# Kernel optimization log

Measured on AMD Instinct MI355X. Metric: run time of the kernel, lower is better.

## Reference

```python
import jax, jax.numpy as jnp
import numpy as np

B, N0, C, K, D = 16384, 1024, 12, 64, 3  # batch, feat dim, num_classes, num_clusters, ndim


def setup_inputs() -> dict:
    key = jax.random.key(0)
    ks = jax.random.split(key, 6)
    s = 0.02  # weight init scale
    return {
        "x": jax.random.normal(ks[0], (B, N0), dtype=jnp.float32),
        "Wfc": jax.random.normal(ks[1], (N0, C), dtype=jnp.float32) * s,
        "bfc": jnp.zeros((C,), dtype=jnp.float32),
        "Wbin": jax.random.normal(ks[2], (C, K, N0), dtype=jnp.float32) * s,
        "bbin": jnp.zeros((C, K), dtype=jnp.float32),
        "Wres": jax.random.normal(ks[3], (C, K, N0, D), dtype=jnp.float32) * s,
        "bres": jnp.zeros((C, K, D), dtype=jnp.float32),
        "centers": jax.random.normal(ks[4], (K, D), dtype=jnp.float32),
    }


def reference(x, Wfc, bfc, Wbin, bbin, Wres, bres, centers):
    # category head
    y0 = x @ Wfc + bfc                                            # [B, C]
    # per-class bin logits (batched over all classes at once)
    ybin = jnp.einsum("bn,ckn->bck", x, Wbin) + bbin              # [B, C, K]
    ind = jnp.argmax(ybin, axis=2)                                # [B, C] selected cluster per class
    # multires path: all (class, cluster) expert residuals, then one-hot select
    yres_all = jnp.einsum("bn,cknd->bckd", x, Wres) + bres        # [B, C, K, D]
    yres = jnp.take_along_axis(
        yres_all, ind[:, :, None, None], axis=2
    ).squeeze(2)                                                  # [B, C, D]
    # gather cluster centers and add residual
    y = centers[ind] + yres                                       # [B, C, D]
    # torch: stack over classes -> [C,B,D]; permute(1,2,0) -> [B, D, C]
    y1 = jnp.transpose(y, (0, 2, 1))                              # [B, D, C]
    return (y0, y1)
```

## Files before the change

### kernel.cpp

```cpp
#include <hip/hip_runtime.h>

typedef unsigned int uint32;
typedef unsigned long long uint64;
typedef unsigned short ushort16;
typedef __attribute__((ext_vector_type(8))) short bf16x8;
typedef __attribute__((ext_vector_type(4))) float f32x4;
typedef __attribute__((ext_vector_type(4))) uint32 u32x4;

#define B_SZ 16384
#define MARGIN 0.012f

__device__ __forceinline__ ushort16 f2bf(float f) {
  uint32 u = __float_as_uint(f);
  u += 0x7fffu + ((u >> 16) & 1u);
  return (ushort16)(u >> 16);
}
__device__ __forceinline__ float bf2f(ushort16 h) { return __uint_as_float(((uint32)h) << 16); }
__device__ __forceinline__ float bflo(uint32 u) { return __uint_as_float(u << 16); }
__device__ __forceinline__ float bfhi(uint32 u) { return __uint_as_float(u & 0xffff0000u); }
__device__ __forceinline__ uint32 pk2(float lo, float hi) {
  return ((uint32)f2bf(hi) << 16) | (uint32)f2bf(lo);
}
__device__ __forceinline__ int dot4(uint32 a, uint32 b, int c) {
#if __has_builtin(__builtin_amdgcn_sdot4)
  return __builtin_amdgcn_sdot4((int)a, (int)b, c, false);
#else
  int s = c;
#pragma unroll
  for (int k = 0; k < 4; ++k)
    s += (int)(char)(a >> (8 * k)) * (int)(char)(b >> (8 * k));
  return s;
#endif
}
__device__ __forceinline__ int q8(float v, float inv) {
  int q = (int)rintf(v * inv);
  return q > 127 ? 127 : (q < -127 ? -127 : q);
}
__device__ __forceinline__ int red16_i(int s) {
  s += __builtin_amdgcn_update_dpp(0, s, 0xB1, 0xF, 0xF, true);
  s += __builtin_amdgcn_update_dpp(0, s, 0x4E, 0xF, 0xF, true);
  s += __builtin_amdgcn_update_dpp(0, s, 0x141, 0xF, 0xF, true);
  s += __builtin_amdgcn_update_dpp(0, s, 0x140, 0xF, 0xF, true);
  return s;
}
#define DPP_D_LEVEL(v, ctrl)                                                        \
  {                                                                                 \
    uint64 u_ = (uint64)__double_as_longlong(v);                                    \
    int lo_ = __builtin_amdgcn_update_dpp(0, (int)(uint32)u_, (ctrl), 0xF, 0xF, true); \
    int hi_ = __builtin_amdgcn_update_dpp(0, (int)(uint32)(u_ >> 32), (ctrl), 0xF, 0xF, true); \
    (v) += __longlong_as_double((long long)(((uint64)(uint32)hi_ << 32) | (uint32)lo_)); \
  }
__device__ __forceinline__ double red16_d(double v) {
  DPP_D_LEVEL(v, 0xB1); DPP_D_LEVEL(v, 0x4E);
  DPP_D_LEVEL(v, 0x141); DPP_D_LEVEL(v, 0x140);
  return v;
}

__global__ __launch_bounds__(256) void prep_all(
    const float* __restrict__ Wfc, const float* __restrict__ Wbin,
    const float* __restrict__ x, ushort16* __restrict__ Wall,
    u32x4* __restrict__ xb) {
  const int blk = blockIdx.x;
  const int t = threadIdx.x;
  if (blk < 3584) {
    int idx = blk * 256 + t;
    int j = idx >> 10, n = idx & 1023;
    float v = 0.f;
    if (j < 12) v = Wfc[n * 12 + j];
    else if (j >= 64 && j < 832) v = Wbin[(size_t)(j - 64) * 1024 + n];
    Wall[idx] = f2bf(v);
  } else {
    int idx = (blk - 3584) * 256 + t;
    const float4* s = (const float4*)x + (size_t)idx * 2;
    float4 a = s[0], b4 = s[1];
    u32x4 o;
    o.x = pk2(a.x, a.y);  o.y = pk2(a.z, a.w);
    o.z = pk2(b4.x, b4.y); o.w = pk2(b4.z, b4.w);
    xb[idx] = o;
  }
}

__global__ void prep_wall_f(const float* __restrict__ Wfc, const float* __restrict__ Wbin,
                            ushort16* __restrict__ Wall) {
  int idx = blockIdx.x * 256 + threadIdx.x;
  int j = idx >> 10, n = idx & 1023;
  float v = 0.f;
  if (j < 12) v = Wfc[n * 12 + j];
  else if (j >= 64 && j < 832) v = Wbin[(size_t)(j - 64) * 1024 + n];
  Wall[idx] = f2bf(v);
}
__global__ void prep_wres(const float* __restrict__ Wres, ushort16* __restrict__ Wres_b) {
  int idx = blockIdx.x * 256 + threadIdx.x;
  int n = idx & 1023;
  int d = (idx >> 10) % 3;
  int ck = idx / 3072;
  Wres_b[idx] = f2bf(Wres[((size_t)ck * 1024 + n) * 3 + d]);
}

template<int XB>
__global__ __launch_bounds__(256) void gemm_mfma(
    const float* __restrict__ x, const ushort16* __restrict__ xb,
    const float* __restrict__ bfc, const float* __restrict__ bbin,
    const ushort16* __restrict__ Wall, ushort16* __restrict__ ybin,
    unsigned char* __restrict__ ind8, uint64* __restrict__ mask64,
    const float* __restrict__ Wres, uint32* __restrict__ wq,
    float* __restrict__ swk, uint32* __restrict__ xq,
    float* __restrict__ sxb, float* __restrict__ out) {
  __shared__ __align__(16) char smem[49152];
  const int t = threadIdx.x;

  if (XB && blockIdx.x >= 1664) {
    const int lane = t & 63;
    const int b = (blockIdx.x - 1664) * 4 + (t >> 6);
    const float4* xr = (const float4*)(x + (size_t)b * 1024 + lane * 16);
    float4 v0 = xr[0], v1 = xr[1], v2 = xr[2], v3 = xr[3];
    float xv[16] = {v0.x, v0.y, v0.z, v0.w, v1.x, v1.y, v1.z, v1.w,
                    v2.x, v2.y, v2.z, v2.w, v3.x, v3.y, v3.z, v3.w};
    float m = 0.f;
#pragma unroll
    for (int i = 0; i < 16; ++i) m = fmaxf(m, fabsf(xv[i]));
    for (int off = 32; off; off >>= 1) m = fmaxf(m, __shfl_xor(m, off));
    float mx = fmaxf(m, 1e-20f);
    float inv = 127.f / mx;
    if (lane == 0) sxb[b] = mx / 127.f;
    u32x4 qv;
#pragma unroll
    for (int q = 0; q < 4; ++q) {
      uint32 u = ((uint32)(unsigned char)(char)q8(xv[4 * q + 0], inv)) |
                 ((uint32)(unsigned char)(char)q8(xv[4 * q + 1], inv)) << 8 |
                 ((uint32)(unsigned char)(char)q8(xv[4 * q + 2], inv)) << 16 |
                 ((uint32)(unsigned char)(char)q8(xv[4 * q + 3], inv)) << 24;
      qv[q] = u;
    }
    ((u32x4*)(xq + (size_t)b * 256))[lane] = qv;
    return;
  }
  if (XB && blockIdx.x >= 896) {
    float* red = (float*)smem;
    const int ck = blockIdx.x - 896;
    const float4* base4 = (const float4*)(Wres + (size_t)ck * 3072);
    float4 v0 = base4[3 * t], v1 = base4[3 * t + 1], v2 = base4[3 * t + 2];
    float vals[12] = {v0.x, v0.y, v0.z, v0.w, v1.x, v1.y, v1.z, v1.w, v2.x, v2.y, v2.z, v2.w};
    float m = 0.f;
#pragma unroll
    for (int i = 0; i < 12; ++i) m = fmaxf(m, fabsf(vals[i]));
    red[t] = m; __syncthreads();
    for (int s = 128; s; s >>= 1) { if (t < s) red[t] = fmaxf(red[t], red[t + s]); __syncthreads(); }
    float mx = fmaxf(red[0], 1e-20f);
    float inv = 127.f / mx;
    if (t == 0) swk[ck] = mx / 127.f;
#pragma unroll
    for (int d = 0; d < 3; ++d) {
      uint32 u = 0;
#pragma unroll
      for (int j = 0; j < 4; ++j)
        u |= ((uint32)(unsigned char)(char)q8(vals[j * 3 + d], inv)) << (8 * j);
      wq[((size_t)(ck * 3 + d) << 8) + t] = u;
    }
    return;
  }

  const int lane = t & 63, wid = t >> 6;
  const int wm = wid & 1, wn = wid >> 1;

  int orig = blockIdx.x;
  int bid = (orig & 7) * 112 + (orig >> 3);
  int nb = bid % 7, mb = bid / 7;
  const int b0 = mb * 128;

  f32x4 acc[4][4];
#pragma unroll
  for (int i = 0; i < 4; ++i)
#pragma unroll
    for (int j = 0; j < 4; ++j) acc[i][j] = (f32x4){0.f, 0.f, 0.f, 0.f};

  const int lr = lane & 15, lq = lane >> 4;

#define GLDS(srcp, dstoff)                                                      \
  __builtin_amdgcn_global_load_lds(                                             \
      (const __attribute__((address_space(1))) uint32*)(srcp),                  \
      (__attribute__((address_space(3))) uint32*)(smem + (dstoff)), 16, 0, 0)

  if (XB) {
    const int gs2 = (lane & 3) ^ ((lane >> 2) & 3);
    const int grw2 = lane >> 2;
    const int ch0 = wid * 2, ch1 = wid * 2 + 1;
    const ushort16* arow0 = xb + (size_t)(b0 + ch0 * 16 + grw2) * 1024 + gs2 * 8;
    const ushort16* arow1 = xb + (size_t)(b0 + ch1 * 16 + grw2) * 1024 + gs2 * 8;
    const ushort16* brow0 = Wall + (size_t)(nb * 128 + ch0 * 16 + grw2) * 1024 + gs2 * 8;
    const ushort16* brow1 = Wall + (size_t)(nb * 128 + ch1 * 16 + grw2) * 1024 + gs2 * 8;

#define STAGE_HALF(h, buf)                                                      \
    {                                                                           \
      int bb_ = (buf) * 16384;                                                  \
      int kc_ = (h) * 32;                                                       \
      GLDS(arow0 + kc_, bb_ + ch0 * 1024);                                      \
      GLDS(arow1 + kc_, bb_ + ch1 * 1024);                                      \
      GLDS(brow0 + kc_, bb_ + 8192 + ch0 * 1024);                               \
      GLDS(brow1 + kc_, bb_ + 8192 + ch1 * 1024);                               \
    }

    STAGE_HALF(0, 0); STAGE_HALF(1, 1);
    const int cbx2 = (lq * 16) ^ ((lr & 3) << 4);
    const int arow_off = (wm * 64 + lr) * 64;
    const int brow_off = (wn * 64 + lr) * 64;
    int rb = 0;
#pragma unroll 1
    for (int h = 0; h < 32; ++h) {
      if (h < 31) asm volatile("s_waitcnt vmcnt(4)" ::: "memory");
      else        asm volatile("s_waitcnt vmcnt(0)" ::: "memory");
      __builtin_amdgcn_s_barrier();
      if (h < 30) {
        int sb = rb + 2; if (sb >= 3) sb -= 3;
        STAGE_HALF(h + 2, sb);
      }
      const char* base = smem + rb * 16384;
      bf16x8 af[4], bfr[4];
#pragma unroll
      for (int i = 0; i < 4; ++i)
        af[i] = *(const bf16x8*)(base + arow_off + i * 1024 + cbx2);
#pragma unroll
      for (int j = 0; j < 4; ++j)
        bfr[j] = *(const bf16x8*)(base + 8192 + brow_off + j * 1024 + cbx2);
#pragma unroll
      for (int i = 0; i < 4; ++i)
#pragma unroll
        for (int j = 0; j < 4; ++j)
          acc[i][j] = __builtin_amdgcn_mfma_f32_16x16x32_bf16(af[i], bfr[j], acc[i][j], 0, 0, 0);
      rb = (rb == 2) ? 0 : rb + 1;
    }
#undef STAGE_HALF
  } else {
    const int fxor = (lr & 7) << 4;
    for (int kc = 0; kc < 1024; kc += 64) {
      __syncthreads();
      const int sxor = ((t >> 3) & 7) << 4;
#pragma unroll
      for (int i = 0; i < 4; ++i) {
        int s = t + i * 256;
        int row = s >> 3, c8 = (s & 7) * 8;
        int dst = row * 128 + ((c8 * 2) ^ sxor);
        const float4* src = (const float4*)(x + (size_t)(b0 + row) * 1024 + kc + c8);
        float4 v0 = src[0], v1 = src[1];
        u32x4 pv;
        pv.x = pk2(v0.x, v0.y); pv.y = pk2(v0.z, v0.w);
        pv.z = pk2(v1.x, v1.y); pv.w = pk2(v1.z, v1.w);
        *(u32x4*)(smem + dst) = pv;
      }
#pragma unroll
      for (int i = 0; i < 4; ++i) {
        int s = t + i * 256;
        int row = s >> 3, c8 = (s & 7) * 8;
        int dst = 16384 + row * 128 + ((c8 * 2) ^ sxor);
        u32x4 v = *(const u32x4*)(Wall + (size_t)(nb * 128 + row) * 1024 + kc + c8);
        *(u32x4*)(smem + dst) = v;
      }
      __syncthreads();
#pragma unroll
      for (int kk = 0; kk < 2; ++kk) {
        int cbx = (kk * 64 + lq * 16) ^ fxor;
        bf16x8 af[4], bfr[4];
#pragma unroll
        for (int i = 0; i < 4; ++i)
          af[i] = *(const bf16x8*)(smem + (wm * 64 + i * 16 + lr) * 128 + cbx);
#pragma unroll
        for (int j = 0; j < 4; ++j)
          bfr[j] = *(const bf16x8*)(smem + 16384 + (wn * 64 + j * 16 + lr) * 128 + cbx);
#pragma unroll
        for (int i = 0; i < 4; ++i)
#pragma unroll
          for (int j = 0; j < 4; ++j)
            acc[i][j] = __builtin_amdgcn_mfma_f32_16x16x32_bf16(af[i], bfr[j], acc[i][j], 0, 0, 0);
      }
    }
  }
#undef GLDS

  const int g = 2 * nb + wn;
  if (g == 0) {
#pragma unroll
    for (int i = 0; i < 4; ++i)
#pragma unroll
      for (int r = 0; r < 4; ++r) {
        int gm = b0 + wm * 64 + i * 16 + lq * 4 + r;
        if (lr < 12) out[(size_t)gm * 12 + lr] = acc[i][0][r] + bfc[lr];
      }
    return;
  }
  if (g > 12) return;
  const int c = g - 1;
  if (XB == 0) {
#pragma unroll
    for (int i = 0; i < 4; ++i)
#pragma unroll
      for (int j = 0; j < 4; ++j)
#pragma unroll
        for (int r = 0; r < 4; ++r) {
          int gm = b0 + wm * 64 + i * 16 + lq * 4 + r;
          int col = j * 16 + lr;
          ybin[((size_t)gm * 12 + c) * 64 + col] = f2bf(acc[i][j][r] + bbin[c * 64 + col]);
        }
    return;
  }
  float bb[4];
#pragma unroll
  for (int j = 0; j < 4; ++j) bb[j] = bbin[c * 64 + j * 16 + lr];
#pragma unroll
  for (int i = 0; i < 4; ++i)
#pragma unroll
    for (int r = 0; r < 4; ++r) {
      float v0 = acc[i][0][r] + bb[0], v1 = acc[i][1][r] + bb[1];
      float v2 = acc[i][2][r] + bb[2], v3 = acc[i][3][r] + bb[3];
      float m1 = v0, m2 = -3.4e38f; int k1 = lr;
      if (v1 > m1) { m2 = m1; m1 = v1; k1 = 16 + lr; } else m2 = fmaxf(m2, v1);
      if (v2 > m1) { m2 = m1; m1 = v2; k1 = 32 + lr; } else m2 = fmaxf(m2, v2);
      if (v3 > m1) { m2 = m1; m1 = v3; k1 = 48 + lr; } else m2 = fmaxf(m2, v3);
#pragma unroll
      for (int off = 1; off < 16; off <<= 1) {
        float om1 = __shfl_xor(m1, off);
        int   ok1 = __shfl_xor(k1, off);
        float om2 = __shfl_xor(m2, off);
        bool take = (om1 > m1) || (om1 == m1 && ok1 < k1);
        float lose = take ? m1 : om1;
        m2 = fmaxf(fmaxf(m2, om2), lose);
        if (take) { m1 = om1; k1 = ok1; }
      }
      float thr = m1 - MARGIN;
      uint64 bl0 = __ballot(v0 >= thr);
      uint64 bl1 = __ballot(v1 >= thr);
      uint64 bl2 = __ballot(v2 >= thr);
      uint64 bl3 = __ballot(v3 >= thr);
      if (lr == 0) {
        int row = wm * 64 + i * 16 + lq * 4 + r;
        uint64 mk = ((bl0 >> (lq * 16)) & 0xffffull) |
                    (((bl1 >> (lq * 16)) & 0xffffull) << 16) |
                    (((bl2 >> (lq * 16)) & 0xffffull) << 32) |
                    (((bl3 >> (lq * 16)) & 0xffffull) << 48);
        int gp = (b0 + row) * 12 + c;
        ind8[gp] = (unsigned char)(k1 | ((m1 - m2 <= MARGIN) ? 128 : 0));
        mask64[gp] = mk;
      }
    }
}

__global__ __launch_bounds__(256) void compact_k(const unsigned char* __restrict__ ind8,
                                                 uint32* __restrict__ cnt,
                                                 uint32* __restrict__ wl) {
  const int b = blockIdx.x * 256 + threadIdx.x;
  const int lane = threadIdx.x & 63;
  const uint32* p = (const uint32*)(ind8 + b * 12);
  uint32 d0 = p[0], d1 = p[1], d2 = p[2];
  uint32 fmask = 0;
#pragma unroll
  for (int j = 0; j < 4; ++j) {
    if ((d0 >> (8 * j)) & 128u) fmask |= 1u << j;
    if ((d1 >> (8 * j)) & 128u) fmask |= 1u << (4 + j);
    if ((d2 >> (8 * j)) & 128u) fmask |= 1u << (8 + j);
  }
  uint32 n_i = (uint32)__popc(fmask);
  uint32 pre = n_i;
  for (int off = 1; off < 64; off <<= 1) {
    uint32 v = __shfl_up(pre, off);
    if (lane >= off) pre += v;
  }
  uint32 total = __shfl(pre, 63);
  uint32 base = 0;
  if (lane == 63 && total) base = atomicAdd(cnt, total);
  base = __shfl(base, 63);
  uint32 off = base + pre - n_i;
  while (fmask) {
    int c = __ffs(fmask) - 1;
    fmask &= fmask - 1;
    wl[off++] = (uint32)(b * 12 + c);
  }
}

__global__ __launch_bounds__(256) void tail_k(
    const float* __restrict__ x, const float* __restrict__ Wbin,
    const float* __restrict__ bbin, const float* __restrict__ bres,
    const float* __restrict__ centers, const unsigned char* __restrict__ ind8,
    const uint64* __restrict__ mask64, const uint32* __restrict__ wq,
    const float* __restrict__ swk, const uint32* __restrict__ xq,
    const float* __restrict__ sxb, const uint32* __restrict__ cnt,
    const uint32* __restrict__ wl, float* __restrict__ out) {
  const int lane = threadIdx.x & 63;
  const int w = threadIdx.x >> 6;
  const int rm = (int)(blockIdx.x % 3u);
  const int rq = (int)(blockIdx.x / 3u);

  if (rm == 0) {
    const uint32 nresc = *cnt;
#pragma unroll 1
    for (uint32 slot = rq * 4 + w; slot < nresc; slot += 32768) {
      const uint32 pp = wl[slot];
      const int b = (int)(pp / 12u), c = (int)(pp % 12u);

      float xv[16];
      const float4* xr = (const float4*)(x + (size_t)b * 1024 + lane * 16);
#pragma unroll
      for (int q = 0; q < 4; ++q) {
        float4 vv = xr[q];
        xv[4 * q] = vv.x; xv[4 * q + 1] = vv.y; xv[4 * q + 2] = vv.z; xv[4 * q + 3] = vv.w;
      }
      const float sx = sxb[b];
      const float inv = (sx > 0.f) ? 1.f / sx : 0.f;
      uint32 xi[4];
#pragma unroll
      for (int q = 0; q < 4; ++q)
        xi[q] = ((uint32)(unsigned char)(char)q8(xv[4 * q + 0], inv)) |
                ((uint32)(unsigned char)(char)q8(xv[4 * q + 1], inv)) << 8 |
                ((uint32)(unsigned char)(char)q8(xv[4 * q + 2], inv)) << 16 |
                ((uint32)(unsigned char)(char)q8(xv[4 * q + 3], inv)) << 24;

      uint64 mask = mask64[pp];
      double best = -1.0e300;
      int bk = 0;
#pragma unroll 1
      while (mask) {
        int kk[4];
        int nc = 0;
        while (mask && nc < 4) { kk[nc++] = __ffsll(mask) - 1; mask &= mask - 1; }
#pragma unroll
        for (int j = 1; j < 4; ++j) if (j >= nc) kk[j] = kk[0];
        double s[4] = {0.0, 0.0, 0.0, 0.0};
#pragma unroll
        for (int ci = 0; ci < 4; ++ci) {
          const float4* wr4 = (const float4*)(Wbin + ((size_t)c * 64 + kk[ci]) * 1024 + lane * 16);
#pragma unroll
          for (int q = 0; q < 4; ++q) {
            float4 wvv = wr4[q];
            s[ci] += (double)xv[4 * q] * (double)wvv.x + (double)xv[4 * q + 1] * (double)wvv.y +
                     (double)xv[4 * q + 2] * (double)wvv.z + (double)xv[4 * q + 3] * (double)wvv.w;
          }
        }
#pragma unroll
        for (int ci = 0; ci < 4; ++ci) s[ci] = red16_d(s[ci]);
        for (int off = 16; off < 64; off <<= 1) {
#pragma unroll
          for (int ci = 0; ci < 4; ++ci) s[ci] += __shfl_xor(s[ci], off);
        }
#pragma unroll
        for (int ci = 0; ci < 4; ++ci) {
          double sv = s[ci] + (double)bbin[c * 64 + kk[ci]];
          if (ci < nc && sv > best) { best = sv; bk = kk[ci]; }
        }
      }
      const int ck = c * 64 + bk;
      const uint32* wr = wq + (size_t)ck * 768;
      int acc[3];
#pragma unroll
      for (int d = 0; d < 3; ++d) {
        u32x4 wvq = *(const u32x4*)(wr + d * 256 + lane * 4);
        int ss = dot4(xi[0], wvq.x, 0);
        ss = dot4(xi[1], wvq.y, ss);
        ss = dot4(xi[2], wvq.z, ss);
        acc[d] = dot4(xi[3], wvq.w, ss);
      }
#pragma unroll
      for (int d = 0; d < 3; ++d) acc[d] = red16_i(acc[d]);
      for (int off = 16; off < 64; off <<= 1) {
        acc[0] += __shfl_xor(acc[0], off);
        acc[1] += __shfl_xor(acc[1], off);
        acc[2] += __shfl_xor(acc[2], off);
      }
      if (lane == 0) {
        const size_t obase = (size_t)B_SZ * 12 + (size_t)b * 36;
        float sc = sx * swk[ck];
        out[obase + 0 * 12 + c] = centers[bk * 3 + 0] + bres[ck * 3 + 0] + sc * (float)acc[0];
        out[obase + 1 * 12 + c] = centers[bk * 3 + 1] + bres[ck * 3 + 1] + sc * (float)acc[1];
        out[obase + 2 * 12 + c] = centers[bk * 3 + 2] + bres[ck * 3 + 2] + sc * (float)acc[2];
      }
    }
    return;
  }

  const int b = rq * 2 + (rm - 1);

  const u32x4 xi = *(const u32x4*)(xq + (size_t)b * 256 + lane * 4);
  const float sx = sxb[b];
  const size_t obase = (size_t)B_SZ * 12 + (size_t)b * 36;

  int iv[3], ind[3], ck[3];
  u32x4 wv[3][3];
#pragma unroll
  for (int cc = 0; cc < 3; ++cc) {
    int c = w * 3 + cc;
    iv[cc] = ind8[b * 12 + c];
    ind[cc] = iv[cc] & 63;
    ck[cc] = c * 64 + ind[cc];
    const uint32* wr = wq + (size_t)ck[cc] * 768;
#pragma unroll
    for (int d = 0; d < 3; ++d)
      wv[cc][d] = *(const u32x4*)(wr + d * 256 + lane * 4);
  }
  int acc[3][3];
#pragma unroll
  for (int cc = 0; cc < 3; ++cc)
#pragma unroll
    for (int d = 0; d < 3; ++d) {
      int s = dot4(xi.x, wv[cc][d].x, 0);
      s = dot4(xi.y, wv[cc][d].y, s);
      s = dot4(xi.z, wv[cc][d].z, s);
      acc[cc][d] = dot4(xi.w, wv[cc][d].w, s);
    }
#pragma unroll
  for (int cc = 0; cc < 3; ++cc)
#pragma unroll
    for (int d = 0; d < 3; ++d)
      acc[cc][d] = red16_i(acc[cc][d]);
  for (int off = 16; off < 64; off <<= 1) {
#pragma unroll
    for (int cc = 0; cc < 3; ++cc)
#pragma unroll
      for (int d = 0; d < 3; ++d)
        acc[cc][d] += __shfl_xor(acc[cc][d], off);
  }
  if (lane == 0) {
#pragma unroll
    for (int cc = 0; cc < 3; ++cc) {
      if (iv[cc] & 128) continue;
      int c = w * 3 + cc;
      float sc = sx * swk[ck[cc]];
      out[obase + 0 * 12 + c] = centers[ind[cc] * 3 + 0] + bres[ck[cc] * 3 + 0] + sc * (float)acc[cc][0];
      out[obase + 1 * 12 + c] = centers[ind[cc] * 3 + 1] + bres[ck[cc] * 3 + 1] + sc * (float)acc[cc][1];
      out[obase + 2 * 12 + c] = centers[ind[cc] * 3 + 2] + bres[ck[cc] * 3 + 2] + sc * (float)acc[cc][2];
    }
  }
}

__global__ __launch_bounds__(256) void select2(
    const float* __restrict__ x, const float* __restrict__ Wbin,
    const float* __restrict__ bbin, const float* __restrict__ bres,
    const float* __restrict__ centers, const ushort16* __restrict__ Wres_b,
    const ushort16* __restrict__ ybin, float* __restrict__ out) {
  const int lane = threadIdx.x & 63;
  const int w = threadIdx.x >> 6;
  const int b = blockIdx.x;
  float xv[16];
  {
    const float4* xr = (const float4*)(x + (size_t)b * 1024 + lane * 16);
#pragma unroll
    for (int q = 0; q < 4; ++q) {
      float4 v = xr[q];
      xv[4 * q] = v.x; xv[4 * q + 1] = v.y; xv[4 * q + 2] = v.z; xv[4 * q + 3] = v.w;
    }
  }
  const size_t obase = (size_t)B_SZ * 12 + (size_t)b * 36;
#pragma unroll 1
  for (int cc = 0; cc < 3; ++cc) {
    const int c = w * 3 + cc;
    float v = bf2f(ybin[((size_t)b * 12 + c) * 64 + lane]);
    float m1 = v, m2 = -3.4e38f;
    int k1 = lane;
    for (int off = 32; off; off >>= 1) {
      float om1 = __shfl_xor(m1, off);
      int   ok1 = __shfl_xor(k1, off);
      float om2 = __shfl_xor(m2, off);
      bool take = (om1 > m1) || (om1 == m1 && ok1 < k1);
      float lose = take ? m1 : om1;
      m2 = fmaxf(fmaxf(m2, om2), lose);
      if (take) { m1 = om1; k1 = ok1; }
    }
    int ind = k1;
    if (m1 - m2 <= MARGIN) {
      unsigned long long mask = __ballot(v >= m1 - MARGIN);
      double best = -1.0e300;
      int bk = 0;
      while (mask) {
        int k = __ffsll(mask) - 1;
        mask &= (mask - 1);
        const float4* wr4 = (const float4*)(Wbin + ((size_t)c * 64 + k) * 1024 + lane * 16);
        double s = 0.0;
#pragma unroll
        for (int q = 0; q < 4; ++q) {
          float4 wv = wr4[q];
          s += (double)xv[4 * q] * (double)wv.x + (double)xv[4 * q + 1] * (double)wv.y +
               (double)xv[4 * q + 2] * (double)wv.z + (double)xv[4 * q + 3] * (double)wv.w;
        }
        for (int off = 32; off; off >>= 1) s += __shfl_xor(s, off);
        s += (double)bbin[c * 64 + k];
        if (s > best) { best = s; bk = k; }
      }
      ind = bk;
    }
    const ushort16* wr = Wres_b + ((size_t)(c * 64 + ind) * 3) * 1024;
    float a[3] = {0.f, 0.f, 0.f};
#pragma unroll
    for (int d = 0; d < 3; ++d) {
      const u32x4* pp = (const u32x4*)(wr + d * 1024 + lane * 16);
      u32x4 w0 = pp[0], w1 = pp[1];
      uint32 uw[8] = {w0.x, w0.y, w0.z, w0.w, w1.x, w1.y, w1.z, w1.w};
#pragma unroll
      for (int q = 0; q < 8; ++q) {
        a[d] = fmaf(xv[2 * q],     bflo(uw[q]), a[d]);
        a[d] = fmaf(xv[2 * q + 1], bfhi(uw[q]), a[d]);
      }
    }
    for (int off = 32; off; off >>= 1) {
      a[0] += __shfl_xor(a[0], off);
      a[1] += __shfl_xor(a[1], off);
      a[2] += __shfl_xor(a[2], off);
    }
    if (lane == 0) {
      int ck = c * 64 + ind;
      out[obase + 0 * 12 + c] = centers[ind * 3 + 0] + bres[ck * 3 + 0] + a[0];
      out[obase + 1 * 12 + c] = centers[ind * 3 + 1] + bres[ck * 3 + 1] + a[1];
      out[obase + 2 * 12 + c] = centers[ind * 3 + 2] + bres[ck * 3 + 2] + a[2];
    }
  }
}

extern "C" void kernel_launch(void* const* d_in, const int* in_sizes, int n_in,
                              void* d_out, int out_size, void* d_ws, size_t ws_size,
                              hipStream_t stream) {
  const float* x       = (const float*)d_in[0];
  const float* Wfc     = (const float*)d_in[1];
  const float* bfc     = (const float*)d_in[2];
  const float* Wbin    = (const float*)d_in[3];
  const float* bbin    = (const float*)d_in[4];
  const float* Wres    = (const float*)d_in[5];
  const float* bres    = (const float*)d_in[6];
  const float* centers = (const float*)d_in[7];
  float* out = (float*)d_out;

  char* ws = (char*)d_ws;
  ushort16* Wall = (ushort16*)ws;
  if (ws_size >= 57151488ull) {
    uint32*        wq     = (uint32*)(ws + 1835008);
    float*         swk    = (float*)(ws + 4194304);
    unsigned char* ind8   = (unsigned char*)(ws + 4197376);
    uint64*        mask64 = (uint64*)(ws + 4393984);
    ushort16*      xb     = (ushort16*)(ws + 5966848);
    uint32*        xq     = (uint32*)(ws + 39521280);
    float*         sxb    = (float*)(ws + 56298496);
    uint32*        cnt    = (uint32*)(ws + 56364032);
    uint32*        wl     = (uint32*)(ws + 56364288);

    hipMemsetAsync(cnt, 0, 4, stream);
    prep_all<<<11776, 256, 0, stream>>>(Wfc, Wbin, x, Wall, (u32x4*)xb);
    gemm_mfma<1><<<5760, 256, 0, stream>>>(x, xb, bfc, bbin, Wall,
                                           (ushort16*)nullptr, ind8, mask64,
                                           Wres, wq, swk, xq, sxb, out);
    compact_k<<<64, 256, 0, stream>>>(ind8, cnt, wl);
    tail_k<<<24576, 256, 0, stream>>>(x, Wbin, bbin, bres, centers, ind8, mask64,
                                      wq, swk, xq, sxb, cnt, wl, out);
  } else {
    ushort16* Wres_b = (ushort16*)(ws + 1835008);
    ushort16* ybin   = (ushort16*)(ws + 6553600);
    prep_wall_f<<<3584, 256, 0, stream>>>(Wfc, Wbin, Wall);
    prep_wres<<<9216, 256, 0, stream>>>(Wres, Wres_b);
    gemm_mfma<0><<<896, 256, 0, stream>>>(x, (const ushort16*)ws, bfc, bbin, Wall,
                                          ybin, (unsigned char*)nullptr,
                                          (uint64*)nullptr, nullptr,
                                          (uint32*)nullptr, (float*)nullptr,
                                          (uint32*)nullptr, (float*)nullptr, out);
    select2<<<B_SZ, 256, 0, stream>>>(x, Wbin, bbin, bres, centers, Wres_b, ybin, out);
  }
}
```

Before: 141.5 us.

## Enlarge GEMM block to 256x128 tile with 512 threads and wave-level Wres quantization

The main GEMM kernel now uses 512-thread blocks, each computing a 256-row by 128-column tile. This halves the number of blocks that reload the same Wall columns and improves B-operand reuse, at the cost of 72KB of dynamic shared memory for three pipeline buffers. The side work is also regrouped: Wres quantization is done per wave with shuffle reductions instead of a block-wide shared-memory reduction, and x quantization handles 8 rows per block. Fewer blocks fit per CU because of the larger LDS footprint, and the fallback path is split into its own kernel.

```diff
diff --git a/kernel.cpp b/kernel.cpp
--- a/kernel.cpp
+++ b/kernel.cpp
@@ -97,21 +97,104 @@
   Wres_b[idx] = f2bf(Wres[((size_t)ck * 1024 + n) * 3 + d]);
 }
 
-template<int XB>
-__global__ __launch_bounds__(256) void gemm_mfma(
+__global__ __launch_bounds__(256) void gemm_fb(
+    const float* __restrict__ x, const float* __restrict__ bfc,
+    const float* __restrict__ bbin, const ushort16* __restrict__ Wall,
+    ushort16* __restrict__ ybin, float* __restrict__ out) {
+  __shared__ __align__(16) char smem[32768];
+  const int t = threadIdx.x;
+  const int lane = t & 63, wid = t >> 6;
+  const int wm = wid & 1, wn = wid >> 1;
+  int orig = blockIdx.x;
+  int bid = (orig & 7) * 112 + (orig >> 3);
+  int nb = bid % 7, mb = bid / 7;
+  const int b0 = mb * 128;
+  f32x4 acc[4][4];
+#pragma unroll
+  for (int i = 0; i < 4; ++i)
+#pragma unroll
+    for (int j = 0; j < 4; ++j) acc[i][j] = (f32x4){0.f, 0.f, 0.f, 0.f};
+  const int lr = lane & 15, lq = lane >> 4;
+  const int fxor = (lr & 7) << 4;
+  for (int kc = 0; kc < 1024; kc += 64) {
+    __syncthreads();
+    const int sxor = ((t >> 3) & 7) << 4;
+#pragma unroll
+    for (int i = 0; i < 4; ++i) {
+      int s = t + i * 256;
+      int row = s >> 3, c8 = (s & 7) * 8;
+      int dst = row * 128 + ((c8 * 2) ^ sxor);
+      const float4* src = (const float4*)(x + (size_t)(b0 + row) * 1024 + kc + c8);
+      float4 v0 = src[0], v1 = src[1];
+      u32x4 pv;
+      pv.x = pk2(v0.x, v0.y); pv.y = pk2(v0.z, v0.w);
+      pv.z = pk2(v1.x, v1.y); pv.w = pk2(v1.z, v1.w);
+      *(u32x4*)(smem + dst) = pv;
+    }
+#pragma unroll
+    for (int i = 0; i < 4; ++i) {
+      int s = t + i * 256;
+      int row = s >> 3, c8 = (s & 7) * 8;
+      int dst = 16384 + row * 128 + ((c8 * 2) ^ sxor);
+      u32x4 v = *(const u32x4*)(Wall + (size_t)(nb * 128 + row) * 1024 + kc + c8);
+      *(u32x4*)(smem + dst) = v;
+    }
+    __syncthreads();
+#pragma unroll
+    for (int kk = 0; kk < 2; ++kk) {
+      int cbx = (kk * 64 + lq * 16) ^ fxor;
+      bf16x8 af[4], bfr[4];
+#pragma unroll
+      for (int i = 0; i < 4; ++i)
+        af[i] = *(const bf16x8*)(smem + (wm * 64 + i * 16 + lr) * 128 + cbx);
+#pragma unroll
+      for (int j = 0; j < 4; ++j)
+        bfr[j] = *(const bf16x8*)(smem + 16384 + (wn * 64 + j * 16 + lr) * 128 + cbx);
+#pragma unroll
+      for (int i = 0; i < 4; ++i)
+#pragma unroll
+        for (int j = 0; j < 4; ++j)
+          acc[i][j] = __builtin_amdgcn_mfma_f32_16x16x32_bf16(af[i], bfr[j], acc[i][j], 0, 0, 0);
+    }
+  }
+  const int g = 2 * nb + wn;
+  if (g == 0) {
+#pragma unroll
+    for (int i = 0; i < 4; ++i)
+#pragma unroll
+      for (int r = 0; r < 4; ++r) {
+        int gm = b0 + wm * 64 + i * 16 + lq * 4 + r;
+        if (lr < 12) out[(size_t)gm * 12 + lr] = acc[i][0][r] + bfc[lr];
+      }
+    return;
+  }
+  if (g > 12) return;
+  const int c = g - 1;
+#pragma unroll
+  for (int i = 0; i < 4; ++i)
+#pragma unroll
+    for (int j = 0; j < 4; ++j)
+#pragma unroll
+      for (int r = 0; r < 4; ++r) {
+        int gm = b0 + wm * 64 + i * 16 + lq * 4 + r;
+        int col = j * 16 + lr;
+        ybin[((size_t)gm * 12 + c) * 64 + col] = f2bf(acc[i][j][r] + bbin[c * 64 + col]);
+      }
+}
+
+__global__ __launch_bounds__(512) void gemm_mega(
     const float* __restrict__ x, const ushort16* __restrict__ xb,
     const float* __restrict__ bfc, const float* __restrict__ bbin,
-    const ushort16* __restrict__ Wall, ushort16* __restrict__ ybin,
-    unsigned char* __restrict__ ind8, uint64* __restrict__ mask64,
-    const float* __restrict__ Wres, uint32* __restrict__ wq,
-    float* __restrict__ swk, uint32* __restrict__ xq,
+    const ushort16* __restrict__ Wall, unsigned char* __restrict__ ind8,
+    uint64* __restrict__ mask64, const float* __restrict__ Wres,
+    uint32* __restrict__ wq, float* __restrict__ swk, uint32* __restrict__ xq,
     float* __restrict__ sxb, float* __restrict__ out) {
-  __shared__ __align__(16) char smem[49152];
+  extern __shared__ __align__(16) char smem[];
   const int t = threadIdx.x;
-
-  if (XB && blockIdx.x >= 1664) {
-    const int lane = t & 63;
-    const int b = (blockIdx.x - 1664) * 4 + (t >> 6);
+  const int lane = t & 63, wid = t >> 6;
+
+  if (blockIdx.x >= 544) {
+    const int b = (blockIdx.x - 544) * 8 + wid;
     const float4* xr = (const float4*)(x + (size_t)b * 1024 + lane * 16);
     float4 v0 = xr[0], v1 = xr[1], v2 = xr[2], v3 = xr[3];
     float xv[16] = {v0.x, v0.y, v0.z, v0.w, v1.x, v1.y, v1.z, v1.w,
@@ -135,38 +218,45 @@
     ((u32x4*)(xq + (size_t)b * 256))[lane] = qv;
     return;
   }
-  if (XB && blockIdx.x >= 896) {
-    float* red = (float*)smem;
-    const int ck = blockIdx.x - 896;
+  if (blockIdx.x >= 448) {
+    const int ck = (blockIdx.x - 448) * 8 + wid;
     const float4* base4 = (const float4*)(Wres + (size_t)ck * 3072);
-    float4 v0 = base4[3 * t], v1 = base4[3 * t + 1], v2 = base4[3 * t + 2];
-    float vals[12] = {v0.x, v0.y, v0.z, v0.w, v1.x, v1.y, v1.z, v1.w, v2.x, v2.y, v2.z, v2.w};
     float m = 0.f;
 #pragma unroll
-    for (int i = 0; i < 12; ++i) m = fmaxf(m, fabsf(vals[i]));
-    red[t] = m; __syncthreads();
-    for (int s = 128; s; s >>= 1) { if (t < s) red[t] = fmaxf(red[t], red[t + s]); __syncthreads(); }
-    float mx = fmaxf(red[0], 1e-20f);
+    for (int it = 0; it < 4; ++it) {
+      int tt = lane + 64 * it;
+      float4 v0 = base4[3 * tt], v1 = base4[3 * tt + 1], v2 = base4[3 * tt + 2];
+      m = fmaxf(m, fmaxf(fmaxf(fabsf(v0.x), fabsf(v0.y)), fmaxf(fabsf(v0.z), fabsf(v0.w))));
+      m = fmaxf(m, fmaxf(fmaxf(fabsf(v1.x), fabsf(v1.y)), fmaxf(fabsf(v1.z), fabsf(v1.w))));
+      m = fmaxf(m, fmaxf(fmaxf(fabsf(v2.x), fabsf(v2.y)), fmaxf(fabsf(v2.z), fabsf(v2.w))));
+    }
+    for (int off = 32; off; off >>= 1) m = fmaxf(m, __shfl_xor(m, off));
+    float mx = fmaxf(m, 1e-20f);
     float inv = 127.f / mx;
-    if (t == 0) swk[ck] = mx / 127.f;
-#pragma unroll
-    for (int d = 0; d < 3; ++d) {
-      uint32 u = 0;
-#pragma unroll
-      for (int j = 0; j < 4; ++j)
-        u |= ((uint32)(unsigned char)(char)q8(vals[j * 3 + d], inv)) << (8 * j);
-      wq[((size_t)(ck * 3 + d) << 8) + t] = u;
+    if (lane == 0) swk[ck] = mx / 127.f;
+#pragma unroll
+    for (int it = 0; it < 4; ++it) {
+      int tt = lane + 64 * it;
+      float4 v0 = base4[3 * tt], v1 = base4[3 * tt + 1], v2 = base4[3 * tt + 2];
+      float vals[12] = {v0.x, v0.y, v0.z, v0.w, v1.x, v1.y, v1.z, v1.w, v2.x, v2.y, v2.z, v2.w};
+#pragma unroll
+      for (int d = 0; d < 3; ++d) {
+        uint32 u = 0;
+#pragma unroll
+        for (int j = 0; j < 4; ++j)
+          u |= ((uint32)(unsigned char)(char)q8(vals[j * 3 + d], inv)) << (8 * j);
+        wq[((size_t)(ck * 3 + d) << 8) + tt] = u;
+      }
     }
     return;
   }
 
-  const int lane = t & 63, wid = t >> 6;
-  const int wm = wid & 1, wn = wid >> 1;
+  const int wm = wid & 3, wn = wid >> 2;
 
   int orig = blockIdx.x;
-  int bid = (orig & 7) * 112 + (orig >> 3);
+  int bid = (orig & 7) * 56 + (orig >> 3);
   int nb = bid % 7, mb = bid / 7;
-  const int b0 = mb * 128;
+  const int b0 = mb * 256;
 
   f32x4 acc[4][4];
 #pragma unroll
@@ -175,105 +265,68 @@
     for (int j = 0; j < 4; ++j) acc[i][j] = (f32x4){0.f, 0.f, 0.f, 0.f};
 
   const int lr = lane & 15, lq = lane >> 4;
+  const int gs2 = (lane & 3) ^ ((lane >> 2) & 3);
+  const int grw2 = lane >> 2;
 
 #define GLDS(srcp, dstoff)                                                      \
   __builtin_amdgcn_global_load_lds(                                             \
       (const __attribute__((address_space(1))) uint32*)(srcp),                  \
       (__attribute__((address_space(3))) uint32*)(smem + (dstoff)), 16, 0, 0)
 
-  if (XB) {
-    const int gs2 = (lane & 3) ^ ((lane >> 2) & 3);
-    const int grw2 = lane >> 2;
-    const int ch0 = wid * 2, ch1 = wid * 2 + 1;
-    const ushort16* arow0 = xb + (size_t)(b0 + ch0 * 16 + grw2) * 1024 + gs2 * 8;
-    const ushort16* arow1 = xb + (size_t)(b0 + ch1 * 16 + grw2) * 1024 + gs2 * 8;
-    const ushort16* brow0 = Wall + (size_t)(nb * 128 + ch0 * 16 + grw2) * 1024 + gs2 * 8;
-    const ushort16* brow1 = Wall + (size_t)(nb * 128 + ch1 * 16 + grw2) * 1024 + gs2 * 8;
+  const ushort16* srcp[3];
+  int dsto[3];
+#pragma unroll
+  for (int k = 0; k < 3; ++k) {
+    int c = wid * 3 + k;
+    if (c < 16) {
+      srcp[k] = xb + (size_t)(b0 + c * 16 + grw2) * 1024 + gs2 * 8;
+      dsto[k] = c * 1024;
+    } else {
+      int cb = c - 16;
+      srcp[k] = Wall + (size_t)(nb * 128 + cb * 16 + grw2) * 1024 + gs2 * 8;
+      dsto[k] = 16384 + cb * 1024;
+    }
+  }
 
 #define STAGE_HALF(h, buf)                                                      \
-    {                                                                           \
-      int bb_ = (buf) * 16384;                                                  \
-      int kc_ = (h) * 32;                                                       \
-      GLDS(arow0 + kc_, bb_ + ch0 * 1024);                                      \
-      GLDS(arow1 + kc_, bb_ + ch1 * 1024);                                      \
-      GLDS(brow0 + kc_, bb_ + 8192 + ch0 * 1024);                               \
-      GLDS(brow1 + kc_, bb_ + 8192 + ch1 * 1024);                               \
-    }
-
-    STAGE_HALF(0, 0); STAGE_HALF(1, 1);
-    const int cbx2 = (lq * 16) ^ ((lr & 3) << 4);
-    const int arow_off = (wm * 64 + lr) * 64;
-    const int brow_off = (wn * 64 + lr) * 64;
-    int rb = 0;
+  {                                                                             \
+    int bb_ = (buf) * 24576;                                                    \
+    int kc_ = (h) * 32;                                                         \
+    GLDS(srcp[0] + kc_, bb_ + dsto[0]);                                         \
+    GLDS(srcp[1] + kc_, bb_ + dsto[1]);                                         \
+    GLDS(srcp[2] + kc_, bb_ + dsto[2]);                                         \
+  }
+
+  STAGE_HALF(0, 0); STAGE_HALF(1, 1);
+  const int cbx2 = (lq * 16) ^ ((lr & 3) << 4);
+  const int arow_off = (wm * 64 + lr) * 64;
+  const int brow_off = (wn * 64 + lr) * 64;
+  int rb = 0;
 #pragma unroll 1
-    for (int h = 0; h < 32; ++h) {
-      if (h < 31) asm volatile("s_waitcnt vmcnt(4)" ::: "memory");
-      else        asm volatile("s_waitcnt vmcnt(0)" ::: "memory");
-      __builtin_amdgcn_s_barrier();
-      if (h < 30) {
-        int sb = rb + 2; if (sb >= 3) sb -= 3;
-        STAGE_HALF(h + 2, sb);
-      }
-      const char* base = smem + rb * 16384;
-      bf16x8 af[4], bfr[4];
-#pragma unroll
-      for (int i = 0; i < 4; ++i)
-        af[i] = *(const bf16x8*)(base + arow_off + i * 1024 + cbx2);
+  for (int h = 0; h < 32; ++h) {
+    if (h < 31) asm volatile("s_waitcnt vmcnt(3)" ::: "memory");
+    else        asm volatile("s_waitcnt vmcnt(0)" ::: "memory");
+    __builtin_amdgcn_s_barrier();
+    if (h < 30) {
+      int sb = rb + 2; if (sb >= 3) sb -= 3;
+      STAGE_HALF(h + 2, sb);
+    }
+    const char* base = smem + rb * 24576;
+    bf16x8 af[4], bfr[4];
+#pragma unroll
+    for (int i = 0; i < 4; ++i)
+      af[i] = *(const bf16x8*)(base + arow_off + i * 1024 + cbx2);
+#pragma unroll
+    for (int j = 0; j < 4; ++j)
+      bfr[j] = *(const bf16x8*)(base + 16384 + brow_off + j * 1024 + cbx2);
+#pragma unroll
+    for (int i = 0; i < 4; ++i)
 #pragma unroll
       for (int j = 0; j < 4; ++j)
-        bfr[j] = *(const bf16x8*)(base + 8192 + brow_off + j * 1024 + cbx2);
-#pragma unroll
-      for (int i = 0; i < 4; ++i)
-#pragma unroll
-        for (int j = 0; j < 4; ++j)
-          acc[i][j] = __builtin_amdgcn_mfma_f32_16x16x32_bf16(af[i], bfr[j], acc[i][j], 0, 0, 0);
-      rb = (rb == 2) ? 0 : rb + 1;
-    }
+        acc[i][j] = __builtin_amdgcn_mfma_f32_16x16x32_bf16(af[i], bfr[j], acc[i][j], 0, 0, 0);
+    rb = (rb == 2) ? 0 : rb + 1;
+  }
 #undef STAGE_HALF
-  } else {
-    const int fxor = (lr & 7) << 4;
-    for (int kc = 0; kc < 1024; kc += 64) {
-      __syncthreads();
-      const int sxor = ((t >> 3) & 7) << 4;
-#pragma unroll
-      for (int i = 0; i < 4; ++i) {
-        int s = t + i * 256;
-        int row = s >> 3, c8 = (s & 7) * 8;
-        int dst = row * 128 + ((c8 * 2) ^ sxor);
-        const float4* src = (const float4*)(x + (size_t)(b0 + row) * 1024 + kc + c8);
-        float4 v0 = src[0], v1 = src[1];
-        u32x4 pv;
-        pv.x = pk2(v0.x, v0.y); pv.y = pk2(v0.z, v0.w);
-        pv.z = pk2(v1.x, v1.y); pv.w = pk2(v1.z, v1.w);
-        *(u32x4*)(smem + dst) = pv;
-      }
-#pragma unroll
-      for (int i = 0; i < 4; ++i) {
-        int s = t + i * 256;
-        int row = s >> 3, c8 = (s & 7) * 8;
-        int dst = 16384 + row * 128 + ((c8 * 2) ^ sxor);
-        u32x4 v = *(const u32x4*)(Wall + (size_t)(nb * 128 + row) * 1024 + kc + c8);
-        *(u32x4*)(smem + dst) = v;
-      }
-      __syncthreads();
-#pragma unroll
-      for (int kk = 0; kk < 2; ++kk) {
-        int cbx = (kk * 64 + lq * 16) ^ fxor;
-        bf16x8 af[4], bfr[4];
-#pragma unroll
-        for (int i = 0; i < 4; ++i)
-          af[i] = *(const bf16x8*)(smem + (wm * 64 + i * 16 + lr) * 128 + cbx);
-#pragma unroll
-        for (int j = 0; j < 4; ++j)
-          bfr[j] = *(const bf16x8*)(smem + 16384 + (wn * 64 + j * 16 + lr) * 128 + cbx);
-#pragma unroll
-        for (int i = 0; i < 4; ++i)
-#pragma unroll
-          for (int j = 0; j < 4; ++j)
-            acc[i][j] = __builtin_amdgcn_mfma_f32_16x16x32_bf16(af[i], bfr[j], acc[i][j], 0, 0, 0);
-      }
-    }
-  }
 #undef GLDS
 
   const int g = 2 * nb + wn;
@@ -289,19 +342,6 @@
   }
   if (g > 12) return;
   const int c = g - 1;
-  if (XB == 0) {
-#pragma unroll
-    for (int i = 0; i < 4; ++i)
-#pragma unroll
-      for (int j = 0; j < 4; ++j)
-#pragma unroll
-        for (int r = 0; r < 4; ++r) {
-          int gm = b0 + wm * 64 + i * 16 + lq * 4 + r;
-          int col = j * 16 + lr;
-          ybin[((size_t)gm * 12 + c) * 64 + col] = f2bf(acc[i][j][r] + bbin[c * 64 + col]);
-        }
-    return;
-  }
   float bb[4];
 #pragma unroll
   for (int j = 0; j < 4; ++j) bb[j] = bbin[c * 64 + j * 16 + lr];
@@ -636,11 +676,12 @@
     uint32*        cnt    = (uint32*)(ws + 56364032);
     uint32*        wl     = (uint32*)(ws + 56364288);
 
+    (void)hipFuncSetAttribute((const void*)gemm_mega,
+                              hipFuncAttributeMaxDynamicSharedMemorySize, 73728);
     hipMemsetAsync(cnt, 0, 4, stream);
     prep_all<<<11776, 256, 0, stream>>>(Wfc, Wbin, x, Wall, (u32x4*)xb);
-    gemm_mfma<1><<<5760, 256, 0, stream>>>(x, xb, bfc, bbin, Wall,
-                                           (ushort16*)nullptr, ind8, mask64,
-                                           Wres, wq, swk, xq, sxb, out);
+    gemm_mega<<<2592, 512, 73728, stream>>>(x, xb, bfc, bbin, Wall, ind8, mask64,
+                                            Wres, wq, swk, xq, sxb, out);
     compact_k<<<64, 256, 0, stream>>>(ind8, cnt, wl);
     tail_k<<<24576, 256, 0, stream>>>(x, Wbin, bbin, bres, centers, ind8, mask64,
                                       wq, swk, xq, sxb, cnt, wl, out);
@@ -649,11 +690,7 @@
     ushort16* ybin   = (ushort16*)(ws + 6553600);
     prep_wall_f<<<3584, 256, 0, stream>>>(Wfc, Wbin, Wall);
     prep_wres<<<9216, 256, 0, stream>>>(Wres, Wres_b);
-    gemm_mfma<0><<<896, 256, 0, stream>>>(x, (const ushort16*)ws, bfc, bbin, Wall,
-                                          ybin, (unsigned char*)nullptr,
-                                          (uint64*)nullptr, nullptr,
-                                          (uint32*)nullptr, (float*)nullptr,
-                                          (uint32*)nullptr, (float*)nullptr, out);
+    gemm_fb<<<896, 256, 0, stream>>>(x, bfc, bbin, Wall, ybin, out);
     select2<<<B_SZ, 256, 0, stream>>>(x, Wbin, bbin, bres, centers, Wres_b, ybin, out);
   }
 }
```

Result: faster. 134.3 us (-5.1%).
